# Performance work log

Measured on AMD Instinct MI355X. Metric: run time of the kernel, lower is better.

## Reference

```python
import jax, jax.numpy as jnp
import numpy as np

B, S, D = 2, 2048, 1024
H = 16
HD = D // H
W = 256  # attention window half-width


def setup_inputs() -> dict:
    key = jax.random.key(0)
    ks = jax.random.split(key, 9)
    scale = 1.0 / np.sqrt(D)
    inp = {
        "x": jax.random.normal(ks[0], (B, S, D), dtype=jnp.float32),
        "Wq": jax.random.normal(ks[1], (D, D), dtype=jnp.float32) * scale,
        "bq": jnp.zeros((D,), dtype=jnp.float32),
        "Wk": jax.random.normal(ks[2], (D, D), dtype=jnp.float32) * scale,
        "bk": jnp.zeros((D,), dtype=jnp.float32),
        "Wv": jax.random.normal(ks[3], (D, D), dtype=jnp.float32) * scale,
        "bv": jnp.zeros((D,), dtype=jnp.float32),
        "Wo": jax.random.normal(ks[4], (D, D), dtype=jnp.float32) * scale,
        "bo": jnp.zeros((D,), dtype=jnp.float32),
    }
    return inp


def reference(x, Wq, bq, Wk, bk, Wv, bv, Wo, bo):
    # Linear projections (torch Linear: x @ W.T + b), split heads -> [B,H,S,HD]
    def proj(W, b):
        y = x @ W.T + b
        return y.reshape(B, S, H, HD).transpose(0, 2, 1, 3)

    q = proj(Wq, bq)
    k = proj(Wk, bk)
    v = proj(Wv, bv)

    scores = jnp.einsum("bhqd,bhkd->bhqk", q, k) / jnp.sqrt(
        jnp.asarray(HD, dtype=jnp.float32))

    # banded local mask: keep |i - j| <= W
    i = jnp.arange(S)[:, None]
    j = jnp.arange(S)[None, :]
    local_mask = jnp.abs(i - j) <= W  # [S,S] bool
    scores = jnp.where(local_mask[None, None], scores, -jnp.inf)

    attn = jax.nn.softmax(scores, axis=-1)  # [B,H,S,S]
    context = jnp.einsum("bhqk,bhkd->bhqd", attn, v)
    context = context.transpose(0, 2, 1, 3).reshape(B, S, D)
    out = context @ Wo.T + bo
    return (out, attn)
```

## Files before the change

### kernel.cpp

```cpp
#include <hip/hip_runtime.h>

#define B_ 2
#define S_ 2048
#define D_ 1024
#define H_ 16
#define HD_ 64

typedef __attribute__((ext_vector_type(8))) short short8;
typedef __attribute__((ext_vector_type(4))) float f32x4;
typedef unsigned short u16;

#define MFMA16(a, b, c) __builtin_amdgcn_mfma_f32_16x16x32_bf16((a), (b), (c), 0, 0, 0)

__device__ __forceinline__ u16 f2bf(float f) {
  union { float f; unsigned u; } v; v.f = f;
  unsigned r = v.u + 0x7FFFu + ((v.u >> 16) & 1u);
  return (u16)(r >> 16);
}
__device__ __forceinline__ float bf2f(u16 h) {
  union { unsigned u; float f; } v; v.u = ((unsigned)h) << 16;
  return v.f;
}

template <int EPI>
__global__ __launch_bounds__(256, 2) void gemm_split(
    const float* __restrict__ A, const float* __restrict__ B0,
    const float* __restrict__ B1, const float* __restrict__ B2,
    const float* __restrict__ bias0, const float* __restrict__ bias1,
    const float* __restrict__ bias2, u16* __restrict__ oh0, u16* __restrict__ ol0,
    u16* __restrict__ oh1, u16* __restrict__ ol1, u16* __restrict__ oh2,
    u16* __restrict__ ol2, float* __restrict__ outf) {
  __shared__ u16 Ah[128][40], Al[128][40], Bh[128][40], Bl[128][40];
  const int tid = threadIdx.x;
  const int lane = tid & 63, wave = tid >> 6;
  const int wr = wave >> 1, wc = wave & 1;
  const int g = lane >> 4, ln = lane & 15;
  const int mbase = blockIdx.y * 128;
  const int nbase_g = blockIdx.x * 128;
  const int which = nbase_g >> 10;
  const int obase = nbase_g & 1023;
  const float* Bm = (which == 0) ? B0 : (which == 1) ? B1 : B2;
  const float* bias = (which == 0) ? bias0 : (which == 1) ? bias1 : bias2;
  u16* oh = (which == 0) ? oh0 : (which == 1) ? oh1 : oh2;
  u16* ol = (which == 0) ? ol0 : (which == 1) ? ol1 : ol2;

  f32x4 acc[4][4];
  {
    f32x4 z = {0.f, 0.f, 0.f, 0.f};
#pragma unroll
    for (int i = 0; i < 4; ++i)
#pragma unroll
      for (int j = 0; j < 4; ++j) acc[i][j] = z;
  }

  for (int kt = 0; kt < 32; ++kt) {
    const int k0 = kt * 32;
#pragma unroll
    for (int i = 0; i < 4; ++i) {
      const int u = tid + i * 256;
      const int row = u >> 3, col = (u & 7) * 4;
      float4 fa = *(const float4*)&A[(size_t)(mbase + row) * 1024 + k0 + col];
      float4 fb = *(const float4*)&Bm[(size_t)(obase + row) * 1024 + k0 + col];
      float av[4] = {fa.x, fa.y, fa.z, fa.w};
      float bv[4] = {fb.x, fb.y, fb.z, fb.w};
      u16 ah4[4], al4[4], bh4[4], bl4[4];
#pragma unroll
      for (int e = 0; e < 4; ++e) {
        ah4[e] = f2bf(av[e]);
        al4[e] = f2bf(av[e] - bf2f(ah4[e]));
        bh4[e] = f2bf(bv[e]);
        bl4[e] = f2bf(bv[e] - bf2f(bh4[e]));
      }
      *(ushort4*)&Ah[row][col] = make_ushort4(ah4[0], ah4[1], ah4[2], ah4[3]);
      *(ushort4*)&Al[row][col] = make_ushort4(al4[0], al4[1], al4[2], al4[3]);
      *(ushort4*)&Bh[row][col] = make_ushort4(bh4[0], bh4[1], bh4[2], bh4[3]);
      *(ushort4*)&Bl[row][col] = make_ushort4(bl4[0], bl4[1], bl4[2], bl4[3]);
    }
    __syncthreads();
    short8 af[4][2], bfr[4][2];
#pragma unroll
    for (int mi = 0; mi < 4; ++mi) {
      const int r = wr * 64 + mi * 16 + ln;
      af[mi][0] = *(const short8*)&Ah[r][g * 8];
      af[mi][1] = *(const short8*)&Al[r][g * 8];
    }
#pragma unroll
    for (int ni = 0; ni < 4; ++ni) {
      const int r = wc * 64 + ni * 16 + ln;
      bfr[ni][0] = *(const short8*)&Bh[r][g * 8];
      bfr[ni][1] = *(const short8*)&Bl[r][g * 8];
    }
#pragma unroll
    for (int mi = 0; mi < 4; ++mi)
#pragma unroll
      for (int ni = 0; ni < 4; ++ni) {
        acc[mi][ni] = MFMA16(af[mi][0], bfr[ni][0], acc[mi][ni]);
        acc[mi][ni] = MFMA16(af[mi][0], bfr[ni][1], acc[mi][ni]);
        acc[mi][ni] = MFMA16(af[mi][1], bfr[ni][0], acc[mi][ni]);
      }
    __syncthreads();
  }

  if constexpr (EPI == 0) {
#pragma unroll
    for (int mi = 0; mi < 4; ++mi)
#pragma unroll
      for (int ni = 0; ni < 4; ++ni) {
        const int nl = obase + wc * 64 + ni * 16 + ln;
        const float bv = bias[nl];
        const int hh = nl >> 6, hd = nl & 63;
#pragma unroll
        for (int reg = 0; reg < 4; ++reg) {
          const int mm = mbase + wr * 64 + mi * 16 + g * 4 + reg;
          const int bb = mm >> 11, ss = mm & 2047;
          const size_t dst = ((((size_t)bb * 16 + hh) * 2048) + ss) * 64 + hd;
          const float val = acc[mi][ni][reg] + bv;
          const u16 hi = f2bf(val);
          oh[dst] = hi;
          ol[dst] = f2bf(val - bf2f(hi));
        }
      }
  } else {
#pragma unroll
    for (int mi = 0; mi < 4; ++mi)
#pragma unroll
      for (int ni = 0; ni < 4; ++ni) {
        const int nl = obase + wc * 64 + ni * 16 + ln;
        const float bv = bias[nl];
#pragma unroll
        for (int reg = 0; reg < 4; ++reg) {
          const int mm = mbase + wr * 64 + mi * 16 + g * 4 + reg;
          outf[(size_t)mm * 1024 + nl] = acc[mi][ni][reg] + bv;
        }
      }
  }
}

__global__ __launch_bounds__(256, 2) void attn_kernel(
    const u16* __restrict__ qh, const u16* __restrict__ ql,
    const u16* __restrict__ kh, const u16* __restrict__ kl,
    const u16* __restrict__ vh, const u16* __restrict__ vl,
    float* __restrict__ attn, float* __restrict__ ctx) {
  __shared__ u16 Plds[32][584];
  __shared__ u16 Vth[64][136], Vtl[64][136];
  __shared__ float red[2][4][32];

  const int tid = threadIdx.x, lane = tid & 63, wave = tid >> 6;
  const int g = lane >> 4, ln = lane & 15;
  int bid = blockIdx.x;
  bid = (bid & 7) * 256 + (bid >> 3);
  const int bh = bid >> 6;
  const int qblk = bid & 63;
  const int b = bh >> 4, h = bh & 15;
  const int i0 = qblk * 32;
  const int j0 = i0 - 256;
  const size_t bh_off = (size_t)bh * S_ * HD_;
  const float NINF = -__builtin_inff();

  short8 qf[2][2][2];
#pragma unroll
  for (int mi = 0; mi < 2; ++mi)
#pragma unroll
    for (int ks = 0; ks < 2; ++ks) {
      const size_t off = bh_off + (size_t)(i0 + mi * 16 + ln) * 64 + ks * 32 + g * 8;
      qf[mi][ks][0] = *(const short8*)(qh + off);
      qf[mi][ks][1] = *(const short8*)(ql + off);
    }

  f32x4 acc[2][9];
  {
    f32x4 z = {0.f, 0.f, 0.f, 0.f};
#pragma unroll
    for (int mi = 0; mi < 2; ++mi)
#pragma unroll
      for (int nn = 0; nn < 9; ++nn) acc[mi][nn] = z;
  }
#pragma unroll
  for (int nn = 0; nn < 9; ++nn) {
    const int c = wave * 144 + nn * 16 + ln;
    const int j = j0 + c;
    const int jc = min(max(j, 0), S_ - 1);
    const u16* kp = kh + bh_off + (size_t)jc * 64 + g * 8;
    const u16* lp = kl + bh_off + (size_t)jc * 64 + g * 8;
    short8 bh0 = *(const short8*)kp;
    short8 bh1 = *(const short8*)(kp + 32);
    short8 bl0 = *(const short8*)lp;
    short8 bl1 = *(const short8*)(lp + 32);
#pragma unroll
    for (int mi = 0; mi < 2; ++mi) {
      f32x4 a = acc[mi][nn];
      a = MFMA16(qf[mi][0][0], bh0, a);
      a = MFMA16(qf[mi][1][0], bh1, a);
      a = MFMA16(qf[mi][0][0], bl0, a);
      a = MFMA16(qf[mi][1][0], bl1, a);
      a = MFMA16(qf[mi][0][1], bh0, a);
      a = MFMA16(qf[mi][1][1], bh1, a);
      acc[mi][nn] = a;
    }
  }

#pragma unroll
  for (int mi = 0; mi < 2; ++mi)
#pragma unroll
    for (int nn = 0; nn < 9; ++nn) {
      const int c = wave * 144 + nn * 16 + ln;
      const int j = j0 + c;
#pragma unroll
      for (int reg = 0; reg < 4; ++reg) {
        const int r = mi * 16 + g * 4 + reg;
        const bool valid = (j >= 0) && (j < S_) && (c >= r) && (c <= r + 512);
        const float s = acc[mi][nn][reg] * 0.125f;
        acc[mi][nn][reg] = valid ? s : NINF;
      }
    }

  float rmax[2][4];
#pragma unroll
  for (int mi = 0; mi < 2; ++mi)
#pragma unroll
    for (int reg = 0; reg < 4; ++reg) {
      float m = NINF;
#pragma unroll
      for (int nn = 0; nn < 9; ++nn) m = fmaxf(m, acc[mi][nn][reg]);
#pragma unroll
      for (int msk = 1; msk < 16; msk <<= 1) m = fmaxf(m, __shfl_xor(m, msk, 64));
      rmax[mi][reg] = m;
    }
  if (ln == 0) {
#pragma unroll
    for (int mi = 0; mi < 2; ++mi)
#pragma unroll
      for (int reg = 0; reg < 4; ++reg) red[0][wave][mi * 16 + g * 4 + reg] = rmax[mi][reg];
  }
  __syncthreads();
  float gmax[2][4];
#pragma unroll
  for (int mi = 0; mi < 2; ++mi)
#pragma unroll
    for (int reg = 0; reg < 4; ++reg) {
      const int r = mi * 16 + g * 4 + reg;
      gmax[mi][reg] = fmaxf(fmaxf(red[0][0][r], red[0][1][r]), fmaxf(red[0][2][r], red[0][3][r]));
    }

  float psum[2][4];
#pragma unroll
  for (int mi = 0; mi < 2; ++mi)
#pragma unroll
    for (int reg = 0; reg < 4; ++reg) psum[mi][reg] = 0.f;
#pragma unroll
  for (int mi = 0; mi < 2; ++mi)
#pragma unroll
    for (int nn = 0; nn < 9; ++nn)
#pragma unroll
      for (int reg = 0; reg < 4; ++reg) {
        const float p = __expf(acc[mi][nn][reg] - gmax[mi][reg]);
        acc[mi][nn][reg] = p;
        psum[mi][reg] += p;
      }
#pragma unroll
  for (int mi = 0; mi < 2; ++mi)
#pragma unroll
    for (int reg = 0; reg < 4; ++reg) {
      float s = psum[mi][reg];
#pragma unroll
      for (int msk = 1; msk < 16; msk <<= 1) s += __shfl_xor(s, msk, 64);
      psum[mi][reg] = s;
    }
  if (ln == 0) {
#pragma unroll
    for (int mi = 0; mi < 2; ++mi)
#pragma unroll
      for (int reg = 0; reg < 4; ++reg) red[1][wave][mi * 16 + g * 4 + reg] = psum[mi][reg];
  }
  __syncthreads();
  float inv[2][4];
#pragma unroll
  for (int mi = 0; mi < 2; ++mi)
#pragma unroll
    for (int reg = 0; reg < 4; ++reg) {
      const int r = mi * 16 + g * 4 + reg;
      inv[mi][reg] = 1.f / (red[1][0][r] + red[1][1][r] + red[1][2][r] + red[1][3][r]);
    }

  float* attn_bh = attn + (size_t)bh * S_ * S_;
#pragma unroll
  for (int mi = 0; mi < 2; ++mi)
#pragma unroll
    for (int nn = 0; nn < 9; ++nn) {
      const int c = wave * 144 + nn * 16 + ln;
      const int j = j0 + c;
#pragma unroll
      for (int reg = 0; reg < 4; ++reg) {
        const int r = mi * 16 + g * 4 + reg;
        const float p = acc[mi][nn][reg] * inv[mi][reg];
        const bool valid = (j >= 0) && (j < S_) && (c >= r) && (c <= r + 512);
        if (valid) attn_bh[(size_t)(i0 + r) * S_ + j] = p;
        Plds[r][c] = f2bf(p);
      }
    }

  {
    const int r = tid >> 3, tt = tid & 7;
    const int i = i0 + r;
    const int lo = max(0, i - 256), hi = min(S_ - 1, i + 256);
    float* rowp = attn_bh + (size_t)i * S_;
    const float4 z4 = make_float4(0.f, 0.f, 0.f, 0.f);
    const int lo4 = lo >> 2;
    for (int x = tt; x < lo4; x += 8) ((float4*)rowp)[x] = z4;
    if (tt == 0)
      for (int jj = lo & ~3; jj < lo; ++jj) rowp[jj] = 0.f;
    const int t0 = hi + 1;
    int t4 = (t0 + 3) & ~3;
    if (t4 > S_) t4 = S_;
    if (tt == 1)
      for (int jj = t0; jj < t4; ++jj) rowp[jj] = 0.f;
    for (int x = (t4 >> 2) + tt; x < S_ / 4; x += 8) ((float4*)rowp)[x] = z4;
  }
  __syncthreads();

  f32x4 ctxa[2];
  {
    f32x4 z = {0.f, 0.f, 0.f, 0.f};
    ctxa[0] = z;
    ctxa[1] = z;
  }
  for (int ch = 0; ch < 5; ++ch) {
    const int cw = (ch == 4) ? 64 : 128;
    for (int u = tid; u < cw * 8; u += 256) {
      const int cc = u >> 3, hd0 = (u & 7) * 8;
      const int j = j0 + ch * 128 + cc;
      const int jc = min(max(j, 0), S_ - 1);
      short8 v8 = *(const short8*)(vh + bh_off + (size_t)jc * 64 + hd0);
      short8 w8 = *(const short8*)(vl + bh_off + (size_t)jc * 64 + hd0);
#pragma unroll
      for (int e = 0; e < 8; ++e) {
        Vth[hd0 + e][cc] = (u16)v8[e];
        Vtl[hd0 + e][cc] = (u16)w8[e];
      }
    }
    __syncthreads();
    const int nks = cw >> 5;
    for (int ks = 0; ks < nks; ++ks) {
      const int kc = ks * 32 + g * 8;
      short8 vbh = *(const short8*)&Vth[wave * 16 + ln][kc];
      short8 vbl = *(const short8*)&Vtl[wave * 16 + ln][kc];
#pragma unroll
      for (int mi = 0; mi < 2; ++mi) {
        short8 pa = *(const short8*)&Plds[mi * 16 + ln][ch * 128 + kc];
        ctxa[mi] = MFMA16(pa, vbh, ctxa[mi]);
        ctxa[mi] = MFMA16(pa, vbl, ctxa[mi]);
      }
    }
    __syncthreads();
  }

#pragma unroll
  for (int mi = 0; mi < 2; ++mi)
#pragma unroll
    for (int reg = 0; reg < 4; ++reg) {
      const int r = mi * 16 + g * 4 + reg;
      const int d = wave * 16 + ln;
      ctx[(size_t)(b * S_ + i0 + r) * 1024 + h * 64 + d] = ctxa[mi][reg];
    }
}

extern "C" void kernel_launch(void* const* d_in, const int* in_sizes, int n_in,
                              void* d_out, int out_size, void* d_ws, size_t ws_size,
                              hipStream_t stream) {
  (void)in_sizes; (void)n_in; (void)out_size; (void)ws_size;
  const float* x  = (const float*)d_in[0];
  const float* Wq = (const float*)d_in[1];
  const float* bq = (const float*)d_in[2];
  const float* Wk = (const float*)d_in[3];
  const float* bk = (const float*)d_in[4];
  const float* Wv = (const float*)d_in[5];
  const float* bv = (const float*)d_in[6];
  const float* Wo = (const float*)d_in[7];
  const float* bo = (const float*)d_in[8];
  float* out = (float*)d_out;
  float* attn = out + (size_t)B_ * S_ * D_;

  const size_t P = (size_t)B_ * H_ * S_ * HD_;
  u16* qh = (u16*)d_ws;
  u16* ql = qh + P;
  u16* kh = ql + P;
  u16* kl = kh + P;
  u16* vh = kl + P;
  u16* vl = vh + P;
  float* ctx = (float*)(vl + P);

  dim3 g1(24, 32);
  gemm_split<0><<<g1, 256, 0, stream>>>(x, Wq, Wk, Wv, bq, bk, bv,
                                        qh, ql, kh, kl, vh, vl, nullptr);
  attn_kernel<<<2048, 256, 0, stream>>>(qh, ql, kh, kl, vh, vl, attn, ctx);
  dim3 g3(8, 32);
  gemm_split<1><<<g3, 256, 0, stream>>>(ctx, Wo, Wo, Wo, bo, bo, bo,
                                        nullptr, nullptr, nullptr, nullptr,
                                        nullptr, nullptr, out);
}
```

Baseline: 906.4 us.

## Pre-split fp32 inputs to bf16 hi/lo and stage GEMM tiles via direct LDS loads

Adds separate kernels that convert x, the weights and the attention context into bf16 hi/lo pairs once, instead of converting every tile inside the GEMM loop. The GEMMs then load bf16 tiles straight into LDS with global_load_lds, and the QKV outputs move into one packed buffer. The V transpose in the attention kernel gets an XOR swizzle to cut LDS bank conflicts. The cost is two extra launches, extra workspace and extra global traffic for the split arrays. The unpadded LDS tiles may also bring new bank conflicts on the fragment reads.

```diff
diff --git a/kernel.cpp b/kernel.cpp
--- a/kernel.cpp
+++ b/kernel.cpp
@@ -5,12 +5,18 @@
 #define D_ 1024
 #define H_ 16
 #define HD_ 64
+#define MSZ 4096
 
 typedef __attribute__((ext_vector_type(8))) short short8;
 typedef __attribute__((ext_vector_type(4))) float f32x4;
 typedef unsigned short u16;
 
 #define MFMA16(a, b, c) __builtin_amdgcn_mfma_f32_16x16x32_bf16((a), (b), (c), 0, 0, 0)
+
+typedef __attribute__((address_space(1))) const unsigned int gu32;
+typedef __attribute__((address_space(3))) unsigned int lu32;
+#define STAGE16(gp, lp) \
+  __builtin_amdgcn_global_load_lds((gu32*)(gp), (lu32*)(lp), 16, 0, 0)
 
 __device__ __forceinline__ u16 f2bf(float f) {
   union { float f; unsigned u; } v; v.f = f;
@@ -22,27 +28,74 @@
   return v.f;
 }
 
+__global__ void split_kernel(const float* __restrict__ x, const float* __restrict__ wq,
+                             const float* __restrict__ wk, const float* __restrict__ wv,
+                             const float* __restrict__ wo, u16* __restrict__ xh,
+                             u16* __restrict__ xl, u16* __restrict__ wch,
+                             u16* __restrict__ wcl, u16* __restrict__ woh,
+                             u16* __restrict__ wol) {
+  const size_t base = (size_t)blockIdx.x * 256 + threadIdx.x;
+#pragma unroll
+  for (int it = 0; it < 4; ++it) {
+    const size_t v = base + (size_t)it * 524288;
+    float4 f;
+    u16 *dh, *dl;
+    size_t off;
+    if (v < 1048576) {
+      f = ((const float4*)x)[v]; dh = xh; dl = xl; off = v;
+    } else if (v < 1310720) {
+      f = ((const float4*)wq)[v - 1048576]; dh = wch; dl = wcl; off = v - 1048576;
+    } else if (v < 1572864) {
+      f = ((const float4*)wk)[v - 1310720]; dh = wch; dl = wcl; off = v - 1048576;
+    } else if (v < 1835008) {
+      f = ((const float4*)wv)[v - 1572864]; dh = wch; dl = wcl; off = v - 1048576;
+    } else {
+      f = ((const float4*)wo)[v - 1835008]; dh = woh; dl = wol; off = v - 1835008;
+    }
+    const float e[4] = {f.x, f.y, f.z, f.w};
+    u16 h4[4], l4[4];
+#pragma unroll
+    for (int q = 0; q < 4; ++q) {
+      h4[q] = f2bf(e[q]);
+      l4[q] = f2bf(e[q] - bf2f(h4[q]));
+    }
+    *(ushort4*)&dh[off * 4] = make_ushort4(h4[0], h4[1], h4[2], h4[3]);
+    *(ushort4*)&dl[off * 4] = make_ushort4(l4[0], l4[1], l4[2], l4[3]);
+  }
+}
+
+__global__ void split_ctx(const float* __restrict__ src, u16* __restrict__ dh,
+                          u16* __restrict__ dl) {
+  const size_t base = (size_t)blockIdx.x * 256 + threadIdx.x;
+#pragma unroll
+  for (int it = 0; it < 2; ++it) {
+    const size_t v = base + (size_t)it * 524288;
+    float4 f = ((const float4*)src)[v];
+    const float e[4] = {f.x, f.y, f.z, f.w};
+    u16 h4[4], l4[4];
+#pragma unroll
+    for (int q = 0; q < 4; ++q) {
+      h4[q] = f2bf(e[q]);
+      l4[q] = f2bf(e[q] - bf2f(h4[q]));
+    }
+    *(ushort4*)&dh[v * 4] = make_ushort4(h4[0], h4[1], h4[2], h4[3]);
+    *(ushort4*)&dl[v * 4] = make_ushort4(l4[0], l4[1], l4[2], l4[3]);
+  }
+}
+
 template <int EPI>
-__global__ __launch_bounds__(256, 2) void gemm_split(
-    const float* __restrict__ A, const float* __restrict__ B0,
-    const float* __restrict__ B1, const float* __restrict__ B2,
-    const float* __restrict__ bias0, const float* __restrict__ bias1,
-    const float* __restrict__ bias2, u16* __restrict__ oh0, u16* __restrict__ ol0,
-    u16* __restrict__ oh1, u16* __restrict__ ol1, u16* __restrict__ oh2,
-    u16* __restrict__ ol2, float* __restrict__ outf) {
-  __shared__ u16 Ah[128][40], Al[128][40], Bh[128][40], Bl[128][40];
-  const int tid = threadIdx.x;
-  const int lane = tid & 63, wave = tid >> 6;
+__global__ __launch_bounds__(256, 2) void gemm_bf(
+    const u16* __restrict__ Ahg, const u16* __restrict__ Alg,
+    const u16* __restrict__ Bhg, const u16* __restrict__ Blg,
+    const float* __restrict__ b0, const float* __restrict__ b1,
+    const float* __restrict__ b2, u16* __restrict__ oh, u16* __restrict__ ol,
+    float* __restrict__ outf) {
+  __shared__ u16 Ah[128 * 32], Al[128 * 32], Bh[128 * 32], Bl[128 * 32];
+  const int tid = threadIdx.x, lane = tid & 63, wave = tid >> 6;
   const int wr = wave >> 1, wc = wave & 1;
   const int g = lane >> 4, ln = lane & 15;
   const int mbase = blockIdx.y * 128;
-  const int nbase_g = blockIdx.x * 128;
-  const int which = nbase_g >> 10;
-  const int obase = nbase_g & 1023;
-  const float* Bm = (which == 0) ? B0 : (which == 1) ? B1 : B2;
-  const float* bias = (which == 0) ? bias0 : (which == 1) ? bias1 : bias2;
-  u16* oh = (which == 0) ? oh0 : (which == 1) ? oh1 : oh2;
-  u16* ol = (which == 0) ? ol0 : (which == 1) ? ol1 : ol2;
+  const int nbase = blockIdx.x * 128;
 
   f32x4 acc[4][4];
   {
@@ -53,67 +106,73 @@
       for (int j = 0; j < 4; ++j) acc[i][j] = z;
   }
 
+  const int srow = wave * 16 + (lane >> 2);
+  const int scol = (lane & 3) * 8;
+  const size_t a0 = (size_t)(mbase + srow) * 1024 + scol;
+  const size_t a1 = a0 + (size_t)64 * 1024;
+  const size_t bo0 = (size_t)(nbase + srow) * 1024 + scol;
+  const size_t bo1 = bo0 + (size_t)64 * 1024;
+  u16* const lA0 = &Ah[(wave * 16) * 32];
+  u16* const lA1 = &Ah[(64 + wave * 16) * 32];
+  u16* const lB0 = &Bh[(wave * 16) * 32];
+  u16* const lB1 = &Bh[(64 + wave * 16) * 32];
+  u16* const lA0l = &Al[(wave * 16) * 32];
+  u16* const lA1l = &Al[(64 + wave * 16) * 32];
+  u16* const lB0l = &Bl[(wave * 16) * 32];
+  u16* const lB1l = &Bl[(64 + wave * 16) * 32];
+
   for (int kt = 0; kt < 32; ++kt) {
     const int k0 = kt * 32;
-#pragma unroll
-    for (int i = 0; i < 4; ++i) {
-      const int u = tid + i * 256;
-      const int row = u >> 3, col = (u & 7) * 4;
-      float4 fa = *(const float4*)&A[(size_t)(mbase + row) * 1024 + k0 + col];
-      float4 fb = *(const float4*)&Bm[(size_t)(obase + row) * 1024 + k0 + col];
-      float av[4] = {fa.x, fa.y, fa.z, fa.w};
-      float bv[4] = {fb.x, fb.y, fb.z, fb.w};
-      u16 ah4[4], al4[4], bh4[4], bl4[4];
-#pragma unroll
-      for (int e = 0; e < 4; ++e) {
-        ah4[e] = f2bf(av[e]);
-        al4[e] = f2bf(av[e] - bf2f(ah4[e]));
-        bh4[e] = f2bf(bv[e]);
-        bl4[e] = f2bf(bv[e] - bf2f(bh4[e]));
-      }
-      *(ushort4*)&Ah[row][col] = make_ushort4(ah4[0], ah4[1], ah4[2], ah4[3]);
-      *(ushort4*)&Al[row][col] = make_ushort4(al4[0], al4[1], al4[2], al4[3]);
-      *(ushort4*)&Bh[row][col] = make_ushort4(bh4[0], bh4[1], bh4[2], bh4[3]);
-      *(ushort4*)&Bl[row][col] = make_ushort4(bl4[0], bl4[1], bl4[2], bl4[3]);
-    }
+    STAGE16(Ahg + a0 + k0, lA0);
+    STAGE16(Ahg + a1 + k0, lA1);
+    STAGE16(Alg + a0 + k0, lA0l);
+    STAGE16(Alg + a1 + k0, lA1l);
+    STAGE16(Bhg + bo0 + k0, lB0);
+    STAGE16(Bhg + bo1 + k0, lB1);
+    STAGE16(Blg + bo0 + k0, lB0l);
+    STAGE16(Blg + bo1 + k0, lB1l);
     __syncthreads();
-    short8 af[4][2], bfr[4][2];
+    short8 af[4][2], bf[4][2];
 #pragma unroll
     for (int mi = 0; mi < 4; ++mi) {
       const int r = wr * 64 + mi * 16 + ln;
-      af[mi][0] = *(const short8*)&Ah[r][g * 8];
-      af[mi][1] = *(const short8*)&Al[r][g * 8];
+      af[mi][0] = *(const short8*)&Ah[r * 32 + g * 8];
+      af[mi][1] = *(const short8*)&Al[r * 32 + g * 8];
     }
 #pragma unroll
     for (int ni = 0; ni < 4; ++ni) {
       const int r = wc * 64 + ni * 16 + ln;
-      bfr[ni][0] = *(const short8*)&Bh[r][g * 8];
-      bfr[ni][1] = *(const short8*)&Bl[r][g * 8];
+      bf[ni][0] = *(const short8*)&Bh[r * 32 + g * 8];
+      bf[ni][1] = *(const short8*)&Bl[r * 32 + g * 8];
     }
 #pragma unroll
     for (int mi = 0; mi < 4; ++mi)
 #pragma unroll
       for (int ni = 0; ni < 4; ++ni) {
-        acc[mi][ni] = MFMA16(af[mi][0], bfr[ni][0], acc[mi][ni]);
-        acc[mi][ni] = MFMA16(af[mi][0], bfr[ni][1], acc[mi][ni]);
-        acc[mi][ni] = MFMA16(af[mi][1], bfr[ni][0], acc[mi][ni]);
+        acc[mi][ni] = MFMA16(af[mi][0], bf[ni][0], acc[mi][ni]);
+        acc[mi][ni] = MFMA16(af[mi][0], bf[ni][1], acc[mi][ni]);
+        acc[mi][ni] = MFMA16(af[mi][1], bf[ni][0], acc[mi][ni]);
       }
     __syncthreads();
   }
 
+  const size_t P = (size_t)B_ * H_ * S_ * HD_;
   if constexpr (EPI == 0) {
 #pragma unroll
     for (int mi = 0; mi < 4; ++mi)
 #pragma unroll
       for (int ni = 0; ni < 4; ++ni) {
-        const int nl = obase + wc * 64 + ni * 16 + ln;
-        const float bv = bias[nl];
-        const int hh = nl >> 6, hd = nl & 63;
+        const int nl3 = nbase + wc * 64 + ni * 16 + ln;
+        const int which = nl3 >> 10;
+        const float* bp = (which == 0) ? b0 : (which == 1) ? b1 : b2;
+        const float bv = bp[nl3 & 1023];
+        const int hh = (nl3 >> 6) & 15, hd = nl3 & 63;
 #pragma unroll
         for (int reg = 0; reg < 4; ++reg) {
           const int mm = mbase + wr * 64 + mi * 16 + g * 4 + reg;
           const int bb = mm >> 11, ss = mm & 2047;
-          const size_t dst = ((((size_t)bb * 16 + hh) * 2048) + ss) * 64 + hd;
+          const size_t dst =
+              (size_t)which * P + (((size_t)bb * 16 + hh) * 2048 + ss) * 64 + hd;
           const float val = acc[mi][ni][reg] + bv;
           const u16 hi = f2bf(val);
           oh[dst] = hi;
@@ -125,8 +184,8 @@
     for (int mi = 0; mi < 4; ++mi)
 #pragma unroll
       for (int ni = 0; ni < 4; ++ni) {
-        const int nl = obase + wc * 64 + ni * 16 + ln;
-        const float bv = bias[nl];
+        const int nl = nbase + wc * 64 + ni * 16 + ln;
+        const float bv = b0[nl];
 #pragma unroll
         for (int reg = 0; reg < 4; ++reg) {
           const int mm = mbase + wr * 64 + mi * 16 + g * 4 + reg;
@@ -324,26 +383,30 @@
     ctxa[0] = z;
     ctxa[1] = z;
   }
+  const int a2 = ((wave * 16 + ln) >> 3) & 3;
   for (int ch = 0; ch < 5; ++ch) {
     const int cw = (ch == 4) ? 64 : 128;
     for (int u = tid; u < cw * 8; u += 256) {
       const int cc = u >> 3, hd0 = (u & 7) * 8;
+      const int sw = (u & 3) << 3;
       const int j = j0 + ch * 128 + cc;
       const int jc = min(max(j, 0), S_ - 1);
       short8 v8 = *(const short8*)(vh + bh_off + (size_t)jc * 64 + hd0);
       short8 w8 = *(const short8*)(vl + bh_off + (size_t)jc * 64 + hd0);
+      const int cs = cc ^ sw;
 #pragma unroll
       for (int e = 0; e < 8; ++e) {
-        Vth[hd0 + e][cc] = (u16)v8[e];
-        Vtl[hd0 + e][cc] = (u16)w8[e];
+        Vth[hd0 + e][cs] = (u16)v8[e];
+        Vtl[hd0 + e][cs] = (u16)w8[e];
       }
     }
     __syncthreads();
     const int nks = cw >> 5;
     for (int ks = 0; ks < nks; ++ks) {
       const int kc = ks * 32 + g * 8;
-      short8 vbh = *(const short8*)&Vth[wave * 16 + ln][kc];
-      short8 vbl = *(const short8*)&Vtl[wave * 16 + ln][kc];
+      const int kcs = kc ^ (a2 << 3);
+      short8 vbh = *(const short8*)&Vth[wave * 16 + ln][kcs];
+      short8 vbl = *(const short8*)&Vtl[wave * 16 + ln][kcs];
 #pragma unroll
       for (int mi = 0; mi < 2; ++mi) {
         short8 pa = *(const short8*)&Plds[mi * 16 + ln][ch * 128 + kc];
@@ -381,20 +444,30 @@
   float* attn = out + (size_t)B_ * S_ * D_;
 
   const size_t P = (size_t)B_ * H_ * S_ * HD_;
-  u16* qh = (u16*)d_ws;
-  u16* ql = qh + P;
-  u16* kh = ql + P;
-  u16* kl = kh + P;
-  u16* vh = kl + P;
-  u16* vl = vh + P;
-  float* ctx = (float*)(vl + P);
+  u16* qkvh = (u16*)d_ws;
+  u16* qkvl = qkvh + 3 * P;
+  float* ctx = (float*)(qkvl + 3 * P);
+  u16* xh = (u16*)(ctx + (size_t)MSZ * 1024);
+  u16* xl = xh + (size_t)MSZ * 1024;
+  u16* wch = xl + (size_t)MSZ * 1024;
+  u16* wcl = wch + 3145728;
+  u16* woh = wcl + 3145728;
+  u16* wol = woh + 1048576;
+  u16* ch  = wol + 1048576;
+  u16* cl  = ch + (size_t)MSZ * 1024;
+
+  split_kernel<<<2048, 256, 0, stream>>>(x, Wq, Wk, Wv, Wo, xh, xl, wch, wcl, woh, wol);
 
   dim3 g1(24, 32);
-  gemm_split<0><<<g1, 256, 0, stream>>>(x, Wq, Wk, Wv, bq, bk, bv,
-                                        qh, ql, kh, kl, vh, vl, nullptr);
-  attn_kernel<<<2048, 256, 0, stream>>>(qh, ql, kh, kl, vh, vl, attn, ctx);
+  gemm_bf<0><<<g1, 256, 0, stream>>>(xh, xl, wch, wcl, bq, bk, bv,
+                                     qkvh, qkvl, nullptr);
+
+  attn_kernel<<<2048, 256, 0, stream>>>(qkvh, qkvl, qkvh + P, qkvl + P,
+                                        qkvh + 2 * P, qkvl + 2 * P, attn, ctx);
+
+  split_ctx<<<2048, 256, 0, stream>>>(ctx, ch, cl);
+
   dim3 g3(8, 32);
-  gemm_split<1><<<g3, 256, 0, stream>>>(ctx, Wo, Wo, Wo, bo, bo, bo,
-                                        nullptr, nullptr, nullptr, nullptr,
-                                        nullptr, nullptr, out);
-}
+  gemm_bf<1><<<g3, 256, 0, stream>>>(ch, cl, woh, wol, bo, bo, bo,
+                                     nullptr, nullptr, out);
+}
```

New measurement: 802.3 us. 11.5% less time.
